# Kernel optimization log

Measured on AMD Instinct MI355X. Metric: run time of the kernel, lower is better.

Reference implementation:

```python
import jax, jax.numpy as jnp
import numpy as np

N = 100000
E = 3200000
IN_C, HID_C, OUT_C = 128, 64, 16
NEG_SLOPE = 0.2


def setup_inputs() -> dict:
    key = jax.random.key(0)
    ks = jax.random.split(key, 12)
    x = jax.random.normal(ks[0], (N, IN_C), dtype=jnp.float32)
    # edges with no self-loops (reference then appends one self-loop per node,
    # matching add_remaining_self_loops on a loop-free graph)
    src = jax.random.randint(ks[1], (E,), 0, N)
    off = jax.random.randint(ks[2], (E,), 1, N)
    dst = (src + off) % N
    edge_index = jnp.stack([src, dst]).astype(jnp.int64)
    W1 = jax.random.normal(ks[3], (IN_C, HID_C), jnp.float32) / np.sqrt(IN_C)
    a_src1 = jax.random.normal(ks[4], (HID_C,), jnp.float32) / np.sqrt(HID_C)
    a_dst1 = jax.random.normal(ks[5], (HID_C,), jnp.float32) / np.sqrt(HID_C)
    b1 = jnp.zeros((HID_C,), jnp.float32)
    W2 = jax.random.normal(ks[6], (HID_C, OUT_C), jnp.float32) / np.sqrt(HID_C)
    a_src2 = jax.random.normal(ks[7], (OUT_C,), jnp.float32) / np.sqrt(OUT_C)
    a_dst2 = jax.random.normal(ks[8], (OUT_C,), jnp.float32) / np.sqrt(OUT_C)
    b2 = jnp.zeros((OUT_C,), jnp.float32)
    return {"x": x, "edge_index": edge_index, "W1": W1, "a_src1": a_src1,
            "a_dst1": a_dst1, "b1": b1, "W2": W2, "a_src2": a_src2,
            "a_dst2": a_dst2, "b2": b2}


def gat_conv(x, src, dst, W, a_src, a_dst, b):
    # x: [N, Cin] -> h: [N, Cout]
    h = x @ W
    # per-node attention halves, then per-edge score e_ij = LeakyReLU(a_s[src]+a_d[dst])
    s = h @ a_src  # [N]
    d = h @ a_dst  # [N]
    e = jax.nn.leaky_relu(s[src] + d[dst], NEG_SLOPE)  # [E']
    # segment softmax over incoming edges of each destination node
    m = jax.ops.segment_max(e, dst, num_segments=N)
    m = jnp.where(jnp.isfinite(m), m, 0.0)
    p = jnp.exp(e - m[dst])
    z = jax.ops.segment_sum(p, dst, num_segments=N)
    coef = p / (z[dst] + 1e-16)  # [E']
    # scatter-aggregate messages h[src] weighted by attention
    out = jax.ops.segment_sum(coef[:, None] * h[src], dst, num_segments=N)
    return out + b


def reference(x, edge_index, W1, a_src1, a_dst1, b1, W2, a_src2, a_dst2, b2):
    # add_remaining_self_loops: input graph has no self-loops, so append all N
    loop = jnp.arange(N, dtype=edge_index.dtype)
    src = jnp.concatenate([edge_index[0], loop])
    dst = jnp.concatenate([edge_index[1], loop])
    h = gat_conv(x, src, dst, W1, a_src1, a_dst1, b1)
    h = jax.nn.relu(h)  # dropout is identity at eval
    h = gat_conv(h, src, dst, W2, a_src2, a_dst2, b2)
    return jax.nn.log_softmax(h, axis=1)
```

## Files before the change

kernel.cpp:

```cpp
#include <hip/hip_runtime.h>
#include <math.h>

#define NEG 0.2f

__device__ __forceinline__ float leaky(float x){ return x >= 0.f ? x : NEG*x; }

__device__ __forceinline__ unsigned short f2b(float f){
    unsigned u = __float_as_uint(f);
    unsigned r = u + 0x7fffu + ((u >> 16) & 1u);
    return (unsigned short)(r >> 16);
}
__device__ __forceinline__ float b2f(unsigned short b){
    return __uint_as_float(((unsigned)b) << 16);
}

__global__ void k_rank(const int* __restrict__ ei, int* __restrict__ cnt,
                       int* __restrict__ rank, int E, int ET){
    int i = blockIdx.x*256 + threadIdx.x;
    if (i >= ET) return;
    int dst = (i < E) ? ei[E + i] : (i - E);
    rank[i] = atomicAdd(&cnt[dst], 1);
}
__global__ void k_scan1(const int* __restrict__ cnt, int* __restrict__ bsum, int n){
    __shared__ int sh[256];
    int b = blockIdx.x, tid = threadIdx.x;
    int start = b*1024, s = 0;
    for (int i = tid; i < 1024; i += 256){ int idx = start+i; s += (idx<n)?cnt[idx]:0; }
    sh[tid]=s; __syncthreads();
    for (int d=128; d>0; d>>=1){ if (tid<d) sh[tid]+=sh[tid+d]; __syncthreads(); }
    if (tid==0) bsum[b]=sh[0];
}
__global__ void k_scan2(int* bsum, int nb){
    if (threadIdx.x==0 && blockIdx.x==0){
        int run=0;
        for (int i=0;i<nb;i++){ int v=bsum[i]; bsum[i]=run; run+=v; }
    }
}
__global__ void k_scan3(const int* __restrict__ cnt, const int* __restrict__ bsum,
                        int* __restrict__ rowptr, int n){
    __shared__ int sh[256];
    int b = blockIdx.x, tid = threadIdx.x;
    int i0 = b*1024 + tid*4;
    int v[4]; int local=0;
    #pragma unroll
    for (int k=0;k<4;k++){ int idx=i0+k; v[k]=(idx<n)?cnt[idx]:0; local+=v[k]; }
    sh[tid]=local; __syncthreads();
    for (int d=1; d<256; d<<=1){
        int t = (tid>=d)? sh[tid-d] : 0;
        __syncthreads();
        sh[tid] += t;
        __syncthreads();
    }
    int off = bsum[b] + sh[tid] - local;
    #pragma unroll
    for (int k=0;k<4;k++){
        int idx = i0+k;
        if (idx < n){
            rowptr[idx]=off; off += v[k];
            if (idx==n-1) rowptr[n]=off;
        }
    }
}

__global__ void k_score(const int* __restrict__ ei, const int* __restrict__ rank,
                        const int* __restrict__ rowptr,
                        const float* __restrict__ s, const float* __restrict__ d,
                        int2* __restrict__ csrp, int E, int ET){
    int i = blockIdx.x*256 + threadIdx.x;
    if (i >= ET) return;
    int src = (i < E) ? ei[i]     : (i - E);
    int dst = (i < E) ? ei[E + i] : (i - E);
    float pv = expf(leaky(s[src] + d[dst]));
    csrp[rowptr[dst] + rank[i]] = make_int2(src, __float_as_int(pv));
}

__global__ __launch_bounds__(256) void g1(const float* __restrict__ x,
        const float* __restrict__ W1, const float* __restrict__ a_src,
        const float* __restrict__ a_dst, unsigned short* __restrict__ h1b,
        float* __restrict__ s1, float* __restrict__ d1, int N)
{
    __shared__ float xsh[64][132];
    __shared__ float wsh[128][64];
    const int tid = threadIdx.x;
    const int rowbase = blockIdx.x * 64;
    #pragma unroll
    for (int i = 0; i < 8; ++i){
        int g = tid + i*256;
        ((float4*)&wsh[0][0])[g] = ((const float4*)W1)[g];
    }
    #pragma unroll
    for (int i = 0; i < 8; ++i){
        int g = tid + i*256;
        int r = g >> 5, c4 = g & 31;
        int grow = rowbase + r;
        float4 v = make_float4(0.f,0.f,0.f,0.f);
        if (grow < N) v = ((const float4*)(x + (size_t)grow*128))[c4];
        *(float4*)&xsh[r][c4*4] = v;
    }
    __syncthreads();
    const int tx = tid & 15, ty = tid >> 4;
    float acc[4][4];
    #pragma unroll
    for (int j=0;j<4;++j){
        #pragma unroll
        for (int c=0;c<4;++c) acc[j][c]=0.f;
    }
    #pragma unroll 4
    for (int k4 = 0; k4 < 32; ++k4){
        float4 xv[4], wv[4];
        #pragma unroll
        for (int j=0;j<4;++j) xv[j] = *(const float4*)&xsh[ty*4+j][k4*4];
        #pragma unroll
        for (int i=0;i<4;++i) wv[i] = *(const float4*)&wsh[k4*4+i][tx*4];
        #pragma unroll
        for (int j=0;j<4;++j){
            float x0=xv[j].x, x1=xv[j].y, x2=xv[j].z, x3=xv[j].w;
            acc[j][0]=fmaf(x0,wv[0].x,acc[j][0]); acc[j][1]=fmaf(x0,wv[0].y,acc[j][1]);
            acc[j][2]=fmaf(x0,wv[0].z,acc[j][2]); acc[j][3]=fmaf(x0,wv[0].w,acc[j][3]);
            acc[j][0]=fmaf(x1,wv[1].x,acc[j][0]); acc[j][1]=fmaf(x1,wv[1].y,acc[j][1]);
            acc[j][2]=fmaf(x1,wv[1].z,acc[j][2]); acc[j][3]=fmaf(x1,wv[1].w,acc[j][3]);
            acc[j][0]=fmaf(x2,wv[2].x,acc[j][0]); acc[j][1]=fmaf(x2,wv[2].y,acc[j][1]);
            acc[j][2]=fmaf(x2,wv[2].z,acc[j][2]); acc[j][3]=fmaf(x2,wv[2].w,acc[j][3]);
            acc[j][0]=fmaf(x3,wv[3].x,acc[j][0]); acc[j][1]=fmaf(x3,wv[3].y,acc[j][1]);
            acc[j][2]=fmaf(x3,wv[3].z,acc[j][2]); acc[j][3]=fmaf(x3,wv[3].w,acc[j][3]);
        }
    }
    const float4 asv = *(const float4*)&a_src[tx*4];
    const float4 adv = *(const float4*)&a_dst[tx*4];
    #pragma unroll
    for (int j=0;j<4;++j){
        int r = rowbase + ty*4 + j;
        float sv = acc[j][0]*asv.x + acc[j][1]*asv.y + acc[j][2]*asv.z + acc[j][3]*asv.w;
        float dv = acc[j][0]*adv.x + acc[j][1]*adv.y + acc[j][2]*adv.z + acc[j][3]*adv.w;
        #pragma unroll
        for (int dd=8; dd>0; dd>>=1){ sv += __shfl_xor(sv, dd, 16); dv += __shfl_xor(dv, dd, 16); }
        if (r < N){
            uint2 pk;
            pk.x = (unsigned)f2b(acc[j][0]) | ((unsigned)f2b(acc[j][1]) << 16);
            pk.y = (unsigned)f2b(acc[j][2]) | ((unsigned)f2b(acc[j][3]) << 16);
            *(uint2*)&h1b[(size_t)r*64 + tx*4] = pk;
            if (tx == 0){ s1[r] = sv; d1[r] = dv; }
        }
    }
}

__global__ __launch_bounds__(256) void a1(const int* __restrict__ rowptr,
        const int2* __restrict__ csrp, const unsigned short* __restrict__ h1b,
        const float* __restrict__ b1, float* __restrict__ out1, int N)
{
    int wid = threadIdx.x>>6, lane = threadIdx.x&63;
    int n = blockIdx.x*4 + wid;
    if (n >= N) return;
    int base = rowptr[n], end = rowptr[n+1];
    float z = 0.f, acc = 0.f;
    #pragma unroll 4
    for (int k = base; k < end; ++k){
        int2 cp = csrp[k];
        float pv = __int_as_float(cp.y);
        z += pv;
        acc = fmaf(pv, b2f(h1b[(size_t)cp.x*64 + lane]), acc);
    }
    out1[(size_t)n*64 + lane] = fmaxf(acc/(z + 1e-16f) + b1[lane], 0.f);
}

__global__ __launch_bounds__(256) void g2(const float* __restrict__ xin,
        const float* __restrict__ W2, const float* __restrict__ a_src,
        const float* __restrict__ a_dst, unsigned short* __restrict__ h2b,
        float* __restrict__ s2, float* __restrict__ d2, int N)
{
    __shared__ float w[64*16];
    const int tid = threadIdx.x;
    for (int k = tid; k < 64*16/4; k += 256)
        ((float4*)w)[k] = ((const float4*)W2)[k];
    __syncthreads();
    int idx = blockIdx.x*256 + tid;
    int n = idx >> 4, c = idx & 15;
    if (n >= N) return;
    const float as = a_src[c], ad = a_dst[c];
    const float4* xr = (const float4*)(xin + (size_t)n*64);
    float acc = 0.f;
    #pragma unroll
    for (int i4 = 0; i4 < 16; ++i4) {
        float4 v = xr[i4];
        acc = fmaf(v.x, w[(i4*4+0)*16 + c], acc);
        acc = fmaf(v.y, w[(i4*4+1)*16 + c], acc);
        acc = fmaf(v.z, w[(i4*4+2)*16 + c], acc);
        acc = fmaf(v.w, w[(i4*4+3)*16 + c], acc);
    }
    h2b[(size_t)n*16 + c] = f2b(acc);
    float sv = acc*as, dv = acc*ad;
    #pragma unroll
    for (int dd = 8; dd > 0; dd >>= 1){ sv += __shfl_xor(sv, dd, 16); dv += __shfl_xor(dv, dd, 16); }
    if (c == 0) { s2[n] = sv; d2[n] = dv; }
}

__global__ __launch_bounds__(256) void a2(const int* __restrict__ rowptr,
        const int2* __restrict__ csrp, const unsigned short* __restrict__ h2b,
        const float* __restrict__ b2, float* __restrict__ out, int N)
{
    int wid = threadIdx.x>>6, lane = threadIdx.x&63;
    int n = blockIdx.x*4 + wid;
    if (n >= N) return;
    int base = rowptr[n], end = rowptr[n+1];
    int c = lane & 15, r = lane >> 4;
    float z = 0.f, acc = 0.f;
    #pragma unroll 2
    for (int k = base + r; k < end; k += 4){
        int2 cp = csrp[k];
        float pv = __int_as_float(cp.y);
        z += pv;
        acc = fmaf(pv, b2f(h2b[(size_t)cp.x*16 + c]), acc);
    }
    acc += __shfl_xor(acc, 16); acc += __shfl_xor(acc, 32);
    z   += __shfl_xor(z, 16);   z   += __shfl_xor(z, 32);
    float o = acc/(z + 1e-16f) + b2[c];
    float mx = o;
    #pragma unroll
    for (int dd=8; dd>0; dd>>=1) mx = fmaxf(mx, __shfl_xor(mx, dd, 16));
    float ex = expf(o - mx);
    float sum = ex;
    #pragma unroll
    for (int dd=8; dd>0; dd>>=1) sum += __shfl_xor(sum, dd, 16);
    if (r == 0) out[(size_t)n*16 + c] = o - mx - logf(sum);
}

extern "C" void kernel_launch(void* const* d_in, const int* in_sizes, int n_in,
                              void* d_out, int out_size, void* d_ws, size_t ws_size,
                              hipStream_t stream)
{
    const float* x      = (const float*)d_in[0];
    const int*   ei     = (const int*)d_in[1];
    const float* W1     = (const float*)d_in[2];
    const float* a_src1 = (const float*)d_in[3];
    const float* a_dst1 = (const float*)d_in[4];
    const float* b1     = (const float*)d_in[5];
    const float* W2     = (const float*)d_in[6];
    const float* a_src2 = (const float*)d_in[7];
    const float* a_dst2 = (const float*)d_in[8];
    const float* b2     = (const float*)d_in[9];
    float* out = (float*)d_out;
    const int N  = in_sizes[0] / 128;
    const int E  = in_sizes[1] / 2;
    const int ET = E + N;

    char* ptr = (char*)d_ws;
    auto alloc = [&](size_t bytes)->char* {
        char* r = ptr; ptr += (bytes + 255) & ~(size_t)255; return r;
    };
    unsigned short* h1b    = (unsigned short*)alloc((size_t)N*64*2);
    unsigned short* h2b    = (unsigned short*)alloc((size_t)N*16*2);
    float*          out1   = (float*)alloc((size_t)N*64*4);
    float*          s1     = (float*)alloc((size_t)N*4);
    float*          d1     = (float*)alloc((size_t)N*4);
    float*          s2     = (float*)alloc((size_t)N*4);
    float*          d2v    = (float*)alloc((size_t)N*4);
    int*            cnt    = (int*)alloc((size_t)N*4);
    int*            rowptr = (int*)alloc((size_t)(N+1)*4);
    int*            rank   = (int*)alloc((size_t)ET*4);
    int2*           csrp   = (int2*)alloc((size_t)ET*8);
    int*            bsum   = (int*)alloc(4096);

    const int gET  = (ET + 255)/256;
    const int nb1  = (N + 1023)/1024;
    const int nbN4 = (N + 3)/4;
    const int gN16 = ((size_t)N*16 + 255)/256;
    const int gG1  = (N + 63)/64;

    hipMemsetAsync(cnt, 0, (size_t)N*4, stream);
    k_rank<<<gET, 256, 0, stream>>>(ei, cnt, rank, E, ET);
    k_scan1<<<nb1, 256, 0, stream>>>(cnt, bsum, N);
    k_scan2<<<1, 64, 0, stream>>>(bsum, nb1);
    k_scan3<<<nb1, 256, 0, stream>>>(cnt, bsum, rowptr, N);

    g1<<<gG1, 256, 0, stream>>>(x, W1, a_src1, a_dst1, h1b, s1, d1, N);
    k_score<<<gET, 256, 0, stream>>>(ei, rank, rowptr, s1, d1, csrp, E, ET);
    a1<<<nbN4, 256, 0, stream>>>(rowptr, csrp, h1b, b1, out1, N);

    g2<<<gN16, 256, 0, stream>>>(out1, W2, a_src2, a_dst2, h2b, s2, d2v, N);
    k_score<<<gET, 256, 0, stream>>>(ei, rank, rowptr, s2, d2v, csrp, E, ET);
    a2<<<nbN4, 256, 0, stream>>>(rowptr, csrp, h2b, b2, out, N);
}
```

Before: 491.2 us.

## Pad degree counters and vectorize aggregation with eight edges per wave in parallel

Spaces the per-node atomic degree counters 64 bytes apart so that concurrent atomics to neighbouring nodes no longer contend on the same cache line. Rewrites both aggregation kernels so each wave processes eight edges at once, with each lane loading 16-byte (layer 1) or 4-byte (layer 2) vectors of bf16 features, followed by a cross-lane shuffle reduction. This aims to raise memory-level parallelism for low-degree gathers. The cost is a 16x larger counter array to memset, strided counter reads in the scan kernels, and extra shuffle work.

```diff
diff --git a/kernel.cpp b/kernel.cpp
--- a/kernel.cpp
+++ b/kernel.cpp
@@ -9,9 +9,6 @@
     unsigned u = __float_as_uint(f);
     unsigned r = u + 0x7fffu + ((u >> 16) & 1u);
     return (unsigned short)(r >> 16);
-}
-__device__ __forceinline__ float b2f(unsigned short b){
-    return __uint_as_float(((unsigned)b) << 16);
 }
 
 __global__ void k_rank(const int* __restrict__ ei, int* __restrict__ cnt,
@@ -19,13 +16,13 @@
     int i = blockIdx.x*256 + threadIdx.x;
     if (i >= ET) return;
     int dst = (i < E) ? ei[E + i] : (i - E);
-    rank[i] = atomicAdd(&cnt[dst], 1);
+    rank[i] = atomicAdd(&cnt[dst << 4], 1);
 }
 __global__ void k_scan1(const int* __restrict__ cnt, int* __restrict__ bsum, int n){
     __shared__ int sh[256];
     int b = blockIdx.x, tid = threadIdx.x;
     int start = b*1024, s = 0;
-    for (int i = tid; i < 1024; i += 256){ int idx = start+i; s += (idx<n)?cnt[idx]:0; }
+    for (int i = tid; i < 1024; i += 256){ int idx = start+i; s += (idx<n)?cnt[idx<<4]:0; }
     sh[tid]=s; __syncthreads();
     for (int d=128; d>0; d>>=1){ if (tid<d) sh[tid]+=sh[tid+d]; __syncthreads(); }
     if (tid==0) bsum[b]=sh[0];
@@ -43,7 +40,7 @@
     int i0 = b*1024 + tid*4;
     int v[4]; int local=0;
     #pragma unroll
-    for (int k=0;k<4;k++){ int idx=i0+k; v[k]=(idx<n)?cnt[idx]:0; local+=v[k]; }
+    for (int k=0;k<4;k++){ int idx=i0+k; v[k]=(idx<n)?cnt[idx<<4]:0; local+=v[k]; }
     sh[tid]=local; __syncthreads();
     for (int d=1; d<256; d<<=1){
         int t = (tid>=d)? sh[tid-d] : 0;
@@ -152,15 +149,43 @@
     int n = blockIdx.x*4 + wid;
     if (n >= N) return;
     int base = rowptr[n], end = rowptr[n+1];
-    float z = 0.f, acc = 0.f;
-    #pragma unroll 4
-    for (int k = base; k < end; ++k){
+    int es = lane >> 3, cg = lane & 7;
+    float a0=0.f,a1v=0.f,a2v=0.f,a3=0.f,a4=0.f,a5=0.f,a6=0.f,a7=0.f;
+    float z = 0.f;
+    for (int k = base + es; k < end; k += 8){
         int2 cp = csrp[k];
         float pv = __int_as_float(cp.y);
         z += pv;
-        acc = fmaf(pv, b2f(h1b[(size_t)cp.x*64 + lane]), acc);
-    }
-    out1[(size_t)n*64 + lane] = fmaxf(acc/(z + 1e-16f) + b1[lane], 0.f);
+        uint4 hv = *(const uint4*)(h1b + (size_t)cp.x*64 + cg*8);
+        a0 = fmaf(pv, __uint_as_float(hv.x << 16),          a0);
+        a1v= fmaf(pv, __uint_as_float(hv.x & 0xffff0000u),  a1v);
+        a2v= fmaf(pv, __uint_as_float(hv.y << 16),          a2v);
+        a3 = fmaf(pv, __uint_as_float(hv.y & 0xffff0000u),  a3);
+        a4 = fmaf(pv, __uint_as_float(hv.z << 16),          a4);
+        a5 = fmaf(pv, __uint_as_float(hv.z & 0xffff0000u),  a5);
+        a6 = fmaf(pv, __uint_as_float(hv.w << 16),          a6);
+        a7 = fmaf(pv, __uint_as_float(hv.w & 0xffff0000u),  a7);
+    }
+    #pragma unroll
+    for (int m = 8; m <= 32; m <<= 1){
+        a0 += __shfl_xor(a0, m); a1v += __shfl_xor(a1v, m);
+        a2v += __shfl_xor(a2v, m); a3 += __shfl_xor(a3, m);
+        a4 += __shfl_xor(a4, m); a5 += __shfl_xor(a5, m);
+        a6 += __shfl_xor(a6, m); a7 += __shfl_xor(a7, m);
+        z  += __shfl_xor(z, m);
+    }
+    if (es == 0){
+        float zi = 1.f/(z + 1e-16f);
+        const float4 b0 = *(const float4*)(b1 + cg*8);
+        const float4 b4 = *(const float4*)(b1 + cg*8 + 4);
+        float4 o0 = make_float4(fmaxf(a0*zi + b0.x, 0.f), fmaxf(a1v*zi + b0.y, 0.f),
+                                fmaxf(a2v*zi + b0.z, 0.f), fmaxf(a3*zi + b0.w, 0.f));
+        float4 o4 = make_float4(fmaxf(a4*zi + b4.x, 0.f), fmaxf(a5*zi + b4.y, 0.f),
+                                fmaxf(a6*zi + b4.z, 0.f), fmaxf(a7*zi + b4.w, 0.f));
+        float* op = out1 + (size_t)n*64 + cg*8;
+        *(float4*)op = o0;
+        *(float4*)(op+4) = o4;
+    }
 }
 
 __global__ __launch_bounds__(256) void g2(const float* __restrict__ xin,
@@ -202,26 +227,34 @@
     int n = blockIdx.x*4 + wid;
     if (n >= N) return;
     int base = rowptr[n], end = rowptr[n+1];
-    int c = lane & 15, r = lane >> 4;
-    float z = 0.f, acc = 0.f;
-    #pragma unroll 2
-    for (int k = base + r; k < end; k += 4){
+    int es = lane >> 3, cg = lane & 7;
+    float a0=0.f, a1v=0.f, z=0.f;
+    for (int k = base + es; k < end; k += 8){
         int2 cp = csrp[k];
         float pv = __int_as_float(cp.y);
         z += pv;
-        acc = fmaf(pv, b2f(h2b[(size_t)cp.x*16 + c]), acc);
-    }
-    acc += __shfl_xor(acc, 16); acc += __shfl_xor(acc, 32);
-    z   += __shfl_xor(z, 16);   z   += __shfl_xor(z, 32);
-    float o = acc/(z + 1e-16f) + b2[c];
-    float mx = o;
-    #pragma unroll
-    for (int dd=8; dd>0; dd>>=1) mx = fmaxf(mx, __shfl_xor(mx, dd, 16));
-    float ex = expf(o - mx);
-    float sum = ex;
-    #pragma unroll
-    for (int dd=8; dd>0; dd>>=1) sum += __shfl_xor(sum, dd, 16);
-    if (r == 0) out[(size_t)n*16 + c] = o - mx - logf(sum);
+        unsigned hv = *(const unsigned*)(h2b + (size_t)cp.x*16 + cg*2);
+        a0 = fmaf(pv, __uint_as_float(hv << 16),         a0);
+        a1v= fmaf(pv, __uint_as_float(hv & 0xffff0000u), a1v);
+    }
+    #pragma unroll
+    for (int m = 8; m <= 32; m <<= 1){
+        a0 += __shfl_xor(a0, m); a1v += __shfl_xor(a1v, m); z += __shfl_xor(z, m);
+    }
+    float zi = 1.f/(z + 1e-16f);
+    float2 bv = *(const float2*)(b2 + cg*2);
+    float o0 = a0*zi + bv.x;
+    float o1 = a1v*zi + bv.y;
+    float mx = fmaxf(o0, o1);
+    #pragma unroll
+    for (int m = 1; m <= 4; m <<= 1) mx = fmaxf(mx, __shfl_xor(mx, m));
+    float sum = expf(o0 - mx) + expf(o1 - mx);
+    #pragma unroll
+    for (int m = 1; m <= 4; m <<= 1) sum += __shfl_xor(sum, m);
+    if (es == 0){
+        float ls = logf(sum);
+        *(float2*)(out + (size_t)n*16 + cg*2) = make_float2(o0 - mx - ls, o1 - mx - ls);
+    }
 }
 
 extern "C" void kernel_launch(void* const* d_in, const int* in_sizes, int n_in,
@@ -254,7 +287,7 @@
     float*          d1     = (float*)alloc((size_t)N*4);
     float*          s2     = (float*)alloc((size_t)N*4);
     float*          d2v    = (float*)alloc((size_t)N*4);
-    int*            cnt    = (int*)alloc((size_t)N*4);
+    int*            cnt    = (int*)alloc((size_t)N*16*4);
     int*            rowptr = (int*)alloc((size_t)(N+1)*4);
     int*            rank   = (int*)alloc((size_t)ET*4);
     int2*           csrp   = (int2*)alloc((size_t)ET*8);
@@ -266,7 +299,7 @@
     const int gN16 = ((size_t)N*16 + 255)/256;
     const int gG1  = (N + 63)/64;
 
-    hipMemsetAsync(cnt, 0, (size_t)N*4, stream);
+    hipMemsetAsync(cnt, 0, (size_t)N*16*4, stream);
     k_rank<<<gET, 256, 0, stream>>>(ei, cnt, rank, E, ET);
     k_scan1<<<nb1, 256, 0, stream>>>(cnt, bsum, N);
     k_scan2<<<1, 64, 0, stream>>>(bsum, nb1);
```

Result: faster. 445.5 us (-9.3%).
